# Kernel optimization log

Hardware: AMD Instinct MI355X
Metric: run time of the kernel (lower is better)

Reference implementation:

```python
import jax, jax.numpy as jnp
import numpy as np

B, T, S, D, H, DK, DV, DFF = 2, 2048, 2048, 1024, 16, 64, 64, 4096
EPS = 1e-5


def layer_norm(x, g, b):
    m = jnp.mean(x, axis=-1, keepdims=True)
    v = jnp.var(x, axis=-1, keepdims=True)
    return (x - m) * jax.lax.rsqrt(v + EPS) * g + b


def mha(q_in, k_in, v_in, Wq, bq, Wk, bk, Wv, bv, Wo, bo, mask):
    # q_in: [B, Lq, D]; k_in/v_in: [B, Lk, D]
    Q = (q_in @ Wq + bq).reshape(q_in.shape[0], -1, H, DK).transpose(0, 2, 1, 3)  # [B,H,Lq,dk]
    K = (k_in @ Wk + bk).reshape(k_in.shape[0], -1, H, DK).transpose(0, 2, 1, 3)
    V = (v_in @ Wv + bv).reshape(v_in.shape[0], -1, H, DV).transpose(0, 2, 1, 3)
    scores = jnp.einsum('bhqd,bhkd->bhqk', Q, K) / jnp.float32(np.sqrt(DK))
    scores = jnp.where(mask == 0, jnp.float32(-1e9), scores)
    attn = jax.nn.softmax(scores, axis=-1)
    out = jnp.einsum('bhqk,bhkd->bhqd', attn, V)
    out = out.transpose(0, 2, 1, 3).reshape(q_in.shape[0], -1, H * DV)
    return out @ Wo + bo


def setup_inputs() -> dict:
    key = jax.random.key(0)
    ks = jax.random.split(key, 16)
    s = 0.02
    inp = {
        'x': jax.random.normal(ks[0], (B, T, D), jnp.float32),
        'encoder_output': jax.random.normal(ks[1], (B, S, D), jnp.float32),
        'lookahead_mask': jnp.tril(jnp.ones((T, T), jnp.int32))[None, None],  # [1,1,T,T]
        'padding_mask': jnp.ones((1, 1, 1, S), jnp.int32),
        # self-attention params
        'sa_Wq': jax.random.normal(ks[2], (D, H * DK), jnp.float32) * s,
        'sa_bq': jnp.zeros((H * DK,), jnp.float32),
        'sa_Wk': jax.random.normal(ks[3], (D, H * DK), jnp.float32) * s,
        'sa_bk': jnp.zeros((H * DK,), jnp.float32),
        'sa_Wv': jax.random.normal(ks[4], (D, H * DV), jnp.float32) * s,
        'sa_bv': jnp.zeros((H * DV,), jnp.float32),
        'sa_Wo': jax.random.normal(ks[5], (H * DV, D), jnp.float32) * s,
        'sa_bo': jnp.zeros((D,), jnp.float32),
        # cross-attention params
        'ca_Wq': jax.random.normal(ks[6], (D, H * DK), jnp.float32) * s,
        'ca_bq': jnp.zeros((H * DK,), jnp.float32),
        'ca_Wk': jax.random.normal(ks[7], (D, H * DK), jnp.float32) * s,
        'ca_bk': jnp.zeros((H * DK,), jnp.float32),
        'ca_Wv': jax.random.normal(ks[8], (D, H * DV), jnp.float32) * s,
        'ca_bv': jnp.zeros((H * DV,), jnp.float32),
        'ca_Wo': jax.random.normal(ks[9], (H * DV, D), jnp.float32) * s,
        'ca_bo': jnp.zeros((D,), jnp.float32),
        # feed-forward params
        'ff_W1': jax.random.normal(ks[10], (D, DFF), jnp.float32) * s,
        'ff_b1': jnp.zeros((DFF,), jnp.float32),
        'ff_W2': jax.random.normal(ks[11], (DFF, D), jnp.float32) * s,
        'ff_b2': jnp.zeros((D,), jnp.float32),
        # layer norms
        'ln1_g': jnp.ones((D,), jnp.float32), 'ln1_b': jnp.zeros((D,), jnp.float32),
        'ln2_g': jnp.ones((D,), jnp.float32), 'ln2_b': jnp.zeros((D,), jnp.float32),
        'ln3_g': jnp.ones((D,), jnp.float32), 'ln3_b': jnp.zeros((D,), jnp.float32),
    }
    return inp


def reference(x, encoder_output, lookahead_mask, padding_mask,
              sa_Wq, sa_bq, sa_Wk, sa_bk, sa_Wv, sa_bv, sa_Wo, sa_bo,
              ca_Wq, ca_bq, ca_Wk, ca_bk, ca_Wv, ca_bv, ca_Wo, ca_bo,
              ff_W1, ff_b1, ff_W2, ff_b2,
              ln1_g, ln1_b, ln2_g, ln2_b, ln3_g, ln3_b):
    attn1 = mha(x, x, x, sa_Wq, sa_bq, sa_Wk, sa_bk, sa_Wv, sa_bv, sa_Wo, sa_bo, lookahead_mask)
    addnorm1 = layer_norm(x + attn1, ln1_g, ln1_b)
    attn2 = mha(addnorm1, encoder_output, encoder_output,
                ca_Wq, ca_bq, ca_Wk, ca_bk, ca_Wv, ca_bv, ca_Wo, ca_bo, padding_mask)
    addnorm2 = layer_norm(addnorm1 + attn2, ln2_g, ln2_b)
    ff = jax.nn.relu(addnorm2 @ ff_W1 + ff_b1) @ ff_W2 + ff_b2
    return layer_norm(addnorm2 + ff, ln3_g, ln3_b)
```

## Files before the change

### kernel.cpp

```cpp
#include <hip/hip_runtime.h>

typedef unsigned short u16;
typedef unsigned int   u32;
typedef __attribute__((ext_vector_type(8)))  __bf16 bf16x8;
typedef __attribute__((ext_vector_type(4)))  float  f32x4;
typedef __attribute__((ext_vector_type(16))) float  f32x16;
typedef __attribute__((ext_vector_type(4)))  unsigned short u16x4;

#define DEV static __device__ __forceinline__

DEV u16 cvt_bf16(float f){
  u32 u = __builtin_bit_cast(u32, f);
  u32 r = (u + 0x7FFFu + ((u >> 16) & 1u)) >> 16;
  return (u16)r;
}

typedef __attribute__((address_space(1))) void* as1p;
typedef __attribute__((address_space(3))) void* as3p;

DEV void gld16(void* lds, const void* g){
  __builtin_amdgcn_global_load_lds((as1p)g, (as3p)lds, 16, 0, 0);
}

DEV f32x4 mfma16(bf16x8 a, bf16x8 b, f32x4 c){
  return __builtin_amdgcn_mfma_f32_16x16x32_bf16(a, b, c, 0, 0, 0);
}
DEV f32x16 mfma32(bf16x8 a, bf16x8 b, f32x16 c){
  return __builtin_amdgcn_mfma_f32_32x32x16_bf16(a, b, c, 0, 0, 0);
}

DEV bf16x8 ld8(const u16* p){ return *(const bf16x8*)p; }

DEV u32 cvtpk(float lo, float hi){
  u32 r; asm("v_cvt_pk_bf16_f32 %0, %1, %2" : "=v"(r) : "v"(lo), "v"(hi)); return r;
}
DEV void perm32swap(u32 &a, u32 &b){
  asm("v_permlane32_swap_b32 %0, %1" : "+v"(a), "+v"(b));
}
DEV bf16x8 frag4(u32 w0,u32 w1,u32 w2,u32 w3){
  union{ u32 w[4]; bf16x8 f; } u; u.w[0]=w0; u.w[1]=w1; u.w[2]=w2; u.w[3]=w3; return u.f;
}

DEV int swz64(int row, int blk){ return row*64 + ((blk ^ (row & 7)) << 3); }
DEV int swz32(int row, int blk){ return row*32 + ((blk ^ (row & 3)) << 3); }

__global__ __launch_bounds__(256) void castk(const float* __restrict__ in,
                                             u16* __restrict__ out, int n4){
  int i = blockIdx.x*256 + threadIdx.x;
  if(i >= n4) return;
  f32x4 v = *(const f32x4*)(in + (size_t)i*4);
  u16x4 o;
  #pragma unroll
  for(int j=0;j<4;j++) o[j] = cvt_bf16(v[j]);
  *(u16x4*)(out + (size_t)i*4) = o;
}

__global__ __launch_bounds__(256) void fcopy(const float* __restrict__ s,
                                             float* __restrict__ d, int n){
  int i = blockIdx.x*256 + threadIdx.x;
  if(i < n) d[i] = s[i];
}

__global__ __launch_bounds__(256) void maskbias(const int* __restrict__ pm,
                                                float* __restrict__ bias, int n){
  int i = blockIdx.x*256 + threadIdx.x;
  if(i < n) bias[i] = pm[i] ? 0.f : -8e9f;
}

__global__ __launch_bounds__(256) void wcast_t(const float* __restrict__ W,
                                               u16* __restrict__ Wt, int K, int N){
  __shared__ u16 tile[64][66];
  const int k0 = blockIdx.x*64, n0 = blockIdx.y*64;
  const int lr = threadIdx.x >> 4, c4 = (threadIdx.x & 15)*4;
  #pragma unroll
  for(int p=0;p<4;p++){
    const int r = lr + p*16;
    f32x4 v = *(const f32x4*)&W[(size_t)(k0+r)*N + n0 + c4];
    #pragma unroll
    for(int j=0;j<4;j++) tile[r][c4+j] = cvt_bf16(v[j]);
  }
  __syncthreads();
  #pragma unroll
  for(int p=0;p<4;p++){
    const int n = lr + p*16;
    u16x4 u;
    #pragma unroll
    for(int j=0;j<4;j++) u[j] = tile[c4+j][n];
    *(u16x4*)&Wt[(size_t)(n0+n)*K + k0 + c4] = u;
  }
}

__global__ __launch_bounds__(256) void vtrans(const u16* __restrict__ V,
                                              u16* __restrict__ Vt, int L, int ld){
  __shared__ u16 tile[64][66];
  const int t0 = blockIdx.x*64;
  const int h = blockIdx.y, b = blockIdx.z;
  const int lr = threadIdx.x >> 4, c4 = (threadIdx.x & 15)*4;
  #pragma unroll
  for(int p=0;p<4;p++){
    const int r = lr + p*16;
    u16x4 v = *(const u16x4*)&V[(size_t)(b*L + t0 + r)*ld + h*64 + c4];
    #pragma unroll
    for(int j=0;j<4;j++) tile[r][c4+j] = v[j];
  }
  __syncthreads();
  #pragma unroll
  for(int p=0;p<4;p++){
    const int d = lr + p*16;
    u16x4 u;
    #pragma unroll
    for(int j=0;j<4;j++) u[j] = tile[c4+j][d];
    *(u16x4*)&Vt[((size_t)((b*16 + h)*64 + d))*L + t0 + c4] = u;
  }
}

template<int OMODE, int BN>
__global__ __launch_bounds__(256, BN==128 ? 3 : 4) void gemm_bt(
    const u16* __restrict__ A, const u16* __restrict__ Bt,
    const float* __restrict__ bias, void* __restrict__ Cout,
    int N, int K)
{
  __shared__ __align__(16) u16 As[2][128*32];
  __shared__ __align__(16) u16 Bs[2][BN*32];
  constexpr int NJ = BN/32;
  const int tid = threadIdx.x, wave = tid>>6, lane = tid&63;
  const int fr = lane&15, fg = lane>>4;
  const int bm = blockIdx.x*128, bn = blockIdx.y*BN;
  const int wm = (wave>>1)*64, wn = (wave&1)*(BN/2);
  const f32x4 z4 = {0.f,0.f,0.f,0.f};
  f32x4 acc[4][NJ];
  #pragma unroll
  for(int i=0;i<4;i++)
    #pragma unroll
    for(int j=0;j<NJ;j++) acc[i][j] = z4;

  const int srA = wave*32 + (lane>>2);
  const int cl_l = (lane&3)*8;
  const int cl_g = ((lane&3) ^ ((lane>>2)&3))*8;
  const int srB = (BN==128) ? srA : (wave*16 + (lane>>2));
  const u16* gA = A  + (size_t)(bm + srA)*K + cl_g;
  const u16* gB = Bt + (size_t)(bn + srB)*K + cl_g;

  auto stage = [&](int p, int ko){
    u16* lA = &As[p][srA*32 + cl_l];
    u16* lB = &Bs[p][srB*32 + cl_l];
    gld16(lA,     gA + ko);
    gld16(lA+512, gA + ko + (size_t)16*K);
    gld16(lB,     gB + ko);
    if(BN==128) gld16(lB+512, gB + ko + (size_t)16*K);
  };

  const int nk = K >> 5;
  stage(0, 0);
  __syncthreads();
  for(int kt=0; kt<nk; ++kt){
    const int cur = kt & 1;
    if(kt+1 < nk) stage(cur^1, (kt+1)*32);
    bf16x8 af[4], bfv[NJ];
    #pragma unroll
    for(int i=0;i<4;i++) af[i] = ld8(&As[cur][swz32(wm + i*16 + fr, fg)]);
    #pragma unroll
    for(int j=0;j<NJ;j++) bfv[j] = ld8(&Bs[cur][swz32(wn + j*16 + fr, fg)]);
    __builtin_amdgcn_s_setprio(1);
    #pragma unroll
    for(int i=0;i<4;i++)
      #pragma unroll
      for(int j=0;j<NJ;j++)
        acc[i][j] = mfma16(af[i], bfv[j], acc[i][j]);
    __builtin_amdgcn_s_setprio(0);
    __syncthreads();
  }

  const int r0 = bm + wm + fg*4;
  const int c0 = bn + wn + fr;
  #pragma unroll
  for(int j=0;j<NJ;j++){
    const int col = c0 + j*16;
    const float bv = bias[col];
    #pragma unroll
    for(int i=0;i<4;i++){
      #pragma unroll
      for(int r=0;r<4;r++){
        const float v = acc[i][j][r] + bv;
        const size_t idx = (size_t)(r0 + i*16 + r)*N + col;
        if(OMODE==0)      ((float*)Cout)[idx] = v;
        else if(OMODE==1) ((u16*)Cout)[idx]   = cvt_bf16(v);
        else              ((u16*)Cout)[idx]   = cvt_bf16(fmaxf(v, 0.f));
      }
    }
  }
}

template<bool CAUSAL>
__global__ __launch_bounds__(256,2) void attn2(
    const u16* __restrict__ Qg, int ldq, const u16* __restrict__ Kg, int ldk,
    const u16* __restrict__ Vt, const float* __restrict__ biasg,
    u16* __restrict__ Og, int Lk)
{
  __shared__ __align__(16) u16 Ks[2][64*64];
  __shared__ __align__(16) u16 Vs[2][64*64];
  const int tid = threadIdx.x, wave = tid>>6, lane = tid&63;
  const int l31 = lane&31, hi = lane>>5;
  const int bid = blockIdx.x;
  const int g   = (bid&7)*4 + ((bid>>3)>>4);
  const int qb  = (bid>>3)&15;
  const int h = g&15, b = g>>4;
  const int qi = CAUSAL ? ((qb&1) ? (15-(qb>>1)) : (qb>>1)) : qb;
  const int q0 = qi*128;
  const int qw = q0 + wave*32;
  const int qrow = qw + l31;

  bf16x8 qf[4];
  {
    const u16* Qp = Qg + (size_t)(b*2048 + qrow)*ldq + h*64;
    #pragma unroll
    for(int c=0;c<4;c++) qf[c] = ld8(Qp + c*16 + hi*8);
  }

  f32x16 o0, o1;
  #pragma unroll
  for(int r=0;r<16;r++){ o0[r]=0.f; o1[r]=0.f; }
  float m = -3e38f, lsum = 0.f;

  const int srow = wave*16 + (lane>>3);
  const int cl_l = (lane&7)*8;
  const int cl_g = ((lane&7) ^ ((lane>>3)&7))*8;
  const u16* Kp = Kg + (size_t)(b*2048 + srow)*ldk + h*64 + cl_g;
  const u16* Vp = Vt + ((size_t)((b*16 + h)*64 + srow))*Lk + cl_g;

  auto stage = [&](int p, int kv0){
    u16* lK = &Ks[p][srow*64 + cl_l];
    u16* lV = &Vs[p][srow*64 + cl_l];
    gld16(lK,     Kp + (size_t)kv0*ldk);
    gld16(lK+512, Kp + (size_t)(kv0+8)*ldk);
    gld16(lV,     Vp + kv0);
    gld16(lV+512, Vp + kv0 + 8*(size_t)Lk);
  };

  const int nkt = CAUSAL ? ((q0+128)>>6) : (Lk>>6);

  stage(0, 0);
  __syncthreads();
  for(int kt=0; kt<nkt; ++kt){
    const int cur = kt & 1;
    const int kv0 = kt*64;
    if(kt+1 < nkt) stage(cur^1, (kt+1)*64);

    if(!CAUSAL || kv0 <= qw+31){
      f32x16 s0, s1;
      #pragma unroll
      for(int r=0;r<16;r++){ s0[r]=0.f; s1[r]=0.f; }
      __builtin_amdgcn_s_setprio(1);
      #pragma unroll
      for(int c=0;c<4;c++){
        bf16x8 k0 = ld8(&Ks[cur][swz64(l31,      2*c+hi)]);
        bf16x8 k1 = ld8(&Ks[cur][swz64(32 + l31, 2*c+hi)]);
        s0 = mfma32(k0, qf[c], s0);
        s1 = mfma32(k1, qf[c], s1);
      }
      __builtin_amdgcn_s_setprio(0);

      float p[32];
      #pragma unroll
      for(int r=0;r<16;r++){ p[r]=s0[r]; p[16+r]=s1[r]; }

      if(CAUSAL){
        if(kv0 + 63 > qw){
          #pragma unroll
          for(int n=0;n<2;n++)
            #pragma unroll
            for(int r=0;r<16;r++){
              const int kc = kv0 + 32*n + (r&3) + 8*(r>>2) + 4*hi;
              if(kc > qrow) p[16*n+r] = -8e9f;
            }
        }
      } else {
        #pragma unroll
        for(int n=0;n<2;n++)
          #pragma unroll
          for(int cq=0;cq<4;cq++){
            f32x4 bv = *(const f32x4*)&biasg[kv0 + 32*n + 8*cq + 4*hi];
            #pragma unroll
            for(int i=0;i<4;i++) p[16*n+4*cq+i] += bv[i];
          }
      }

      float pm = p[0];
      #pragma unroll
      for(int r=1;r<32;r++) pm = fmaxf(pm, p[r]);
      pm = fmaxf(pm, __shfl_xor(pm, 32));
      if(__any(pm > m + 8.f)){
        const float nm = fmaxf(m, pm);
        const float fac = __expf((m - nm)*0.125f);
        lsum *= fac;
        #pragma unroll
        for(int r=0;r<16;r++){
          const int qidx = (r&3) + 8*(r>>2) + 4*hi;
          const float fb = __builtin_bit_cast(float,
              __builtin_amdgcn_ds_bpermute(qidx<<2, __builtin_bit_cast(int, fac)));
          o0[r] *= fb; o1[r] *= fb;
        }
        m = nm;
      }
      const float ms = m*0.125f;
      float rs = 0.f;
      #pragma unroll
      for(int r=0;r<32;r++){ p[r] = __expf(p[r]*0.125f - ms); rs += p[r]; }
      rs += __shfl_xor(rs, 32);
      lsum += rs;

      u32 pw[16];
      #pragma unroll
      for(int n=0;n<2;n++)
        #pragma unroll
        for(int cp=0;cp<2;cp++){
          const int base = 16*n + 8*cp, cc = 2*n + cp;
          u32 a1 = cvtpk(p[base+0], p[base+1]);
          u32 a2 = cvtpk(p[base+2], p[base+3]);
          u32 b1 = cvtpk(p[base+4], p[base+5]);
          u32 b2 = cvtpk(p[base+6], p[base+7]);
          perm32swap(a1, b1);
          perm32swap(a2, b2);
          pw[4*cc+0]=a1; pw[4*cc+1]=a2; pw[4*cc+2]=b1; pw[4*cc+3]=b2;
        }

      __builtin_amdgcn_s_setprio(1);
      #pragma unroll
      for(int cc=0;cc<4;cc++){
        bf16x8 pf = frag4(pw[4*cc], pw[4*cc+1], pw[4*cc+2], pw[4*cc+3]);
        bf16x8 v0 = ld8(&Vs[cur][swz64(l31,      2*cc+hi)]);
        bf16x8 v1 = ld8(&Vs[cur][swz64(32 + l31, 2*cc+hi)]);
        o0 = mfma32(pf, v0, o0);
        o1 = mfma32(pf, v1, o1);
      }
      __builtin_amdgcn_s_setprio(0);
    }
    __syncthreads();
  }

  const float invl = 1.f / lsum;
  u16* Op = Og + (size_t)(b*2048 + qw)*1024 + h*64;
  #pragma unroll
  for(int r=0;r<16;r++){
    const int qidx = (r&3) + 8*(r>>2) + 4*hi;
    const float il = __builtin_bit_cast(float,
        __builtin_amdgcn_ds_bpermute(qidx<<2, __builtin_bit_cast(int, invl)));
    Op[(size_t)qidx*1024 + l31]      = cvt_bf16(o0[r]*il);
    Op[(size_t)qidx*1024 + 32 + l31] = cvt_bf16(o1[r]*il);
  }
}

__global__ __launch_bounds__(256) void add_ln(const float* __restrict__ X,
                        const float* __restrict__ Dl,
                        const float* __restrict__ gam, const float* __restrict__ bet,
                        float* __restrict__ outf, u16* __restrict__ outb){
  __shared__ float red[8];
  const int tid = threadIdx.x, wave = tid>>6, lane = tid&63;
  const size_t base = ((size_t)blockIdx.x << 10) + tid*4;
  f32x4 xv = *(const f32x4*)(X + base);
  f32x4 dv = *(const f32x4*)(Dl + base);
  f32x4 v;
  #pragma unroll
  for(int j=0;j<4;j++) v[j] = xv[j] + dv[j];
  float s = v[0]+v[1]+v[2]+v[3];
  float q = v[0]*v[0]+v[1]*v[1]+v[2]*v[2]+v[3]*v[3];
  #pragma unroll
  for(int off=1;off<64;off<<=1){ s += __shfl_xor(s,off); q += __shfl_xor(q,off); }
  if(lane==0){ red[wave]=s; red[4+wave]=q; }
  __syncthreads();
  s = red[0]+red[1]+red[2]+red[3];
  q = red[4]+red[5]+red[6]+red[7];
  const float mean = s*(1.f/1024.f);
  const float var  = q*(1.f/1024.f) - mean*mean;
  const float rr = rsqrtf(var + 1e-5f);
  const int c = tid*4;
  f32x4 y;
  #pragma unroll
  for(int j=0;j<4;j++) y[j] = (v[j]-mean)*rr*gam[c+j] + bet[c+j];
  *(f32x4*)(outf + base) = y;
  if(outb){
    u16x4 ob;
    #pragma unroll
    for(int j=0;j<4;j++) ob[j] = cvt_bf16(y[j]);
    *(u16x4*)(outb + base) = ob;
  }
}

extern "C" void kernel_launch(void* const* d_in, const int* in_sizes, int n_in,
                              void* d_out, int out_size, void* d_ws, size_t ws_size,
                              hipStream_t stream)
{
  (void)in_sizes; (void)n_in; (void)out_size; (void)ws_size;
  const float* x    = (const float*)d_in[0];
  const float* enc  = (const float*)d_in[1];
  const int*   pmask= (const int*)d_in[3];
  const float* saWq = (const float*)d_in[4];  const float* sabq = (const float*)d_in[5];
  const float* saWk = (const float*)d_in[6];  const float* sabk = (const float*)d_in[7];
  const float* saWv = (const float*)d_in[8];  const float* sabv = (const float*)d_in[9];
  const float* saWo = (const float*)d_in[10]; const float* sabo = (const float*)d_in[11];
  const float* caWq = (const float*)d_in[12]; const float* cabq = (const float*)d_in[13];
  const float* caWk = (const float*)d_in[14]; const float* cabk = (const float*)d_in[15];
  const float* caWv = (const float*)d_in[16]; const float* cabv = (const float*)d_in[17];
  const float* caWo = (const float*)d_in[18]; const float* cabo = (const float*)d_in[19];
  const float* fW1  = (const float*)d_in[20]; const float* fb1  = (const float*)d_in[21];
  const float* fW2  = (const float*)d_in[22]; const float* fb2  = (const float*)d_in[23];
  const float* l1g  = (const float*)d_in[24]; const float* l1b  = (const float*)d_in[25];
  const float* l2g  = (const float*)d_in[26]; const float* l2b  = (const float*)d_in[27];
  const float* l3g  = (const float*)d_in[28]; const float* l3b  = (const float*)d_in[29];

  char* wsp = (char*)d_ws;
  size_t off = 0;
  auto take = [&](size_t bytes)->void*{ void* p = wsp + off; off += (bytes + 255) & ~(size_t)255; return p; };
  u16* slotA  = (u16*)take(8388608);
  u16* Encb   = (u16*)take(8388608);
  u16* WqkvT  = (u16*)take(6291456);
  u16* cWqT   = (u16*)take(2097152);
  u16* cWkvT  = (u16*)take(4194304);
  u16* WoT    = (u16*)take(2097152);
  u16* cWoT   = (u16*)take(2097152);
  u16* W1T    = (u16*)take(8388608);
  u16* W2T    = (u16*)take(8388608);
  float* bqkv = (float*)take(16384);
  float* bkvc = (float*)take(16384);
  float* biasg= (float*)take(16384);
  u16* slotB  = (u16*)take(25165824);
  u16* Vtb    = (u16*)take(8388608);
  u16* Ob     = (u16*)take(8388608);
  u16* an1b   = (u16*)take(8388608);
  float* projf= (float*)take(16777216);
  float* an1f = (float*)take(16777216);
  float* an2f = (float*)take(16777216);
  u16* ffh    = (u16*)take(33554432);
  u16* Xbf = slotA;  u16* Qcb = slotA;  u16* an2b = slotA;
  u16* QKVb = slotB; u16* KVc = slotB;

  castk<<<4096,256,0,stream>>>(x,   Xbf,  1048576);
  castk<<<4096,256,0,stream>>>(enc, Encb, 1048576);
  wcast_t<<<dim3(16,16),256,0,stream>>>(saWq, WqkvT,                1024, 1024);
  wcast_t<<<dim3(16,16),256,0,stream>>>(saWk, WqkvT + 1024*1024,    1024, 1024);
  wcast_t<<<dim3(16,16),256,0,stream>>>(saWv, WqkvT + 2*1024*1024,  1024, 1024);
  wcast_t<<<dim3(16,16),256,0,stream>>>(saWo, WoT, 1024, 1024);
  wcast_t<<<dim3(16,16),256,0,stream>>>(caWq, cWqT, 1024, 1024);
  wcast_t<<<dim3(16,16),256,0,stream>>>(caWk, cWkvT,               1024, 1024);
  wcast_t<<<dim3(16,16),256,0,stream>>>(caWv, cWkvT + 1024*1024,   1024, 1024);
  wcast_t<<<dim3(16,16),256,0,stream>>>(caWo, cWoT, 1024, 1024);
  wcast_t<<<dim3(16,64),256,0,stream>>>(fW1, W1T, 1024, 4096);
  wcast_t<<<dim3(64,16),256,0,stream>>>(fW2, W2T, 4096, 1024);
  fcopy<<<4,256,0,stream>>>(sabq, bqkv,        1024);
  fcopy<<<4,256,0,stream>>>(sabk, bqkv + 1024, 1024);
  fcopy<<<4,256,0,stream>>>(sabv, bqkv + 2048, 1024);
  fcopy<<<4,256,0,stream>>>(cabk, bkvc,        1024);
  fcopy<<<4,256,0,stream>>>(cabv, bkvc + 1024, 1024);
  maskbias<<<8,256,0,stream>>>(pmask, biasg, 2048);

  gemm_bt<1,128><<<dim3(32,24),256,0,stream>>>(Xbf, WqkvT, bqkv, QKVb, 3072, 1024);
  vtrans<<<dim3(32,16,2),256,0,stream>>>(QKVb + 2048, Vtb, 2048, 3072);
  attn2<true><<<512,256,0,stream>>>(QKVb, 3072, QKVb + 1024, 3072, Vtb, nullptr, Ob, 2048);
  gemm_bt<0,64><<<dim3(32,16),256,0,stream>>>(Ob, WoT, sabo, projf, 1024, 1024);
  add_ln<<<4096,256,0,stream>>>(x, projf, l1g, l1b, an1f, an1b);

  gemm_bt<1,64><<<dim3(32,16),256,0,stream>>>(an1b, cWqT, cabq, Qcb, 1024, 1024);
  gemm_bt<1,128><<<dim3(32,16),256,0,stream>>>(Encb, cWkvT, bkvc, KVc, 2048, 1024);
  vtrans<<<dim3(32,16,2),256,0,stream>>>(KVc + 1024, Vtb, 2048, 2048);
  attn2<false><<<512,256,0,stream>>>(Qcb, 1024, KVc, 2048, Vtb, biasg, Ob, 2048);
  gemm_bt<0,64><<<dim3(32,16),256,0,stream>>>(Ob, cWoT, cabo, projf, 1024, 1024);
  add_ln<<<4096,256,0,stream>>>(an1f, projf, l2g, l2b, an2f, an2b);

  gemm_bt<2,128><<<dim3(32,32),256,0,stream>>>(an2b, W1T, fb1, ffh, 4096, 1024);
  gemm_bt<0,64><<<dim3(32,16),256,0,stream>>>(ffh, W2T, fb2, projf, 1024, 4096);
  add_ln<<<4096,256,0,stream>>>(an2f, projf, l3g, l3b, (float*)d_out, nullptr);
}
```

Measured before the change: 460.1 us.

## Split attention KV range in two and merge partial results in a combine kernel

```diff
diff --git a/kernel.cpp b/kernel.cpp
--- a/kernel.cpp
+++ b/kernel.cpp
@@ -9,6 +9,8 @@
 
 #define DEV static __device__ __forceinline__
 
+#define SC 0.1803368801111243f
+
 DEV u16 cvt_bf16(float f){
   u32 u = __builtin_bit_cast(u32, f);
   u32 r = (u + 0x7FFFu + ((u >> 16) & 1u)) >> 16;
@@ -30,6 +32,10 @@
 }
 
 DEV bf16x8 ld8(const u16* p){ return *(const bf16x8*)p; }
+
+DEV float vexp2(float x){
+  float y; asm("v_exp_f32 %0, %1" : "=v"(y) : "v"(x)); return y;
+}
 
 DEV u32 cvtpk(float lo, float hi){
   u32 r; asm("v_cvt_pk_bf16_f32 %0, %1, %2" : "=v"(r) : "v"(lo), "v"(hi)); return r;
@@ -192,18 +198,21 @@
 }
 
 template<bool CAUSAL>
-__global__ __launch_bounds__(256,2) void attn2(
+__global__ __launch_bounds__(256,4) void attn3(
     const u16* __restrict__ Qg, int ldq, const u16* __restrict__ Kg, int ldk,
     const u16* __restrict__ Vt, const float* __restrict__ biasg,
-    u16* __restrict__ Og, int Lk)
+    float* __restrict__ Opart, float* __restrict__ Ml, float* __restrict__ Ll,
+    int Lk)
 {
   __shared__ __align__(16) u16 Ks[2][64*64];
   __shared__ __align__(16) u16 Vs[2][64*64];
+  __shared__ float FacL[4][32];
   const int tid = threadIdx.x, wave = tid>>6, lane = tid&63;
   const int l31 = lane&31, hi = lane>>5;
   const int bid = blockIdx.x;
-  const int g   = (bid&7)*4 + ((bid>>3)>>4);
-  const int qb  = (bid>>3)&15;
+  const int g    = (bid&7)*4 + (bid>>8);
+  const int r5   = (bid>>3)&31;
+  const int part = r5&1, qb = r5>>1;
   const int h = g&15, b = g>>4;
   const int qi = CAUSAL ? ((qb&1) ? (15-(qb>>1)) : (qb>>1)) : qb;
   const int q0 = qi*128;
@@ -237,14 +246,15 @@
     gld16(lV+512, Vp + kv0 + 8*(size_t)Lk);
   };
 
-  const int nkt = CAUSAL ? ((q0+128)>>6) : (Lk>>6);
-
-  stage(0, 0);
+  const int span = CAUSAL ? (qi+1) : ((Lk>>6)>>1);
+  const int t0 = part*span, t1 = t0 + span;
+
+  stage(0, t0*64);
   __syncthreads();
-  for(int kt=0; kt<nkt; ++kt){
-    const int cur = kt & 1;
+  for(int kt=t0; kt<t1; ++kt){
+    const int cur = (kt-t0)&1;
     const int kv0 = kt*64;
-    if(kt+1 < nkt) stage(cur^1, (kt+1)*64);
+    if(kt+1 < t1) stage(cur^1, (kt+1)*64);
 
     if(!CAUSAL || kv0 <= qw+31){
       f32x16 s0, s1;
@@ -289,23 +299,22 @@
       #pragma unroll
       for(int r=1;r<32;r++) pm = fmaxf(pm, p[r]);
       pm = fmaxf(pm, __shfl_xor(pm, 32));
-      if(__any(pm > m + 8.f)){
+      if(__any(pm > m + 64.f)){
         const float nm = fmaxf(m, pm);
-        const float fac = __expf((m - nm)*0.125f);
+        const float fac = vexp2((m - nm)*SC);
         lsum *= fac;
+        FacL[wave][l31] = fac;
         #pragma unroll
         for(int r=0;r<16;r++){
           const int qidx = (r&3) + 8*(r>>2) + 4*hi;
-          const float fb = __builtin_bit_cast(float,
-              __builtin_amdgcn_ds_bpermute(qidx<<2, __builtin_bit_cast(int, fac)));
+          const float fb = FacL[wave][qidx];
           o0[r] *= fb; o1[r] *= fb;
         }
         m = nm;
       }
-      const float ms = m*0.125f;
       float rs = 0.f;
       #pragma unroll
-      for(int r=0;r<32;r++){ p[r] = __expf(p[r]*0.125f - ms); rs += p[r]; }
+      for(int r=0;r<32;r++){ p[r] = vexp2((p[r]-m)*SC); rs += p[r]; }
       rs += __shfl_xor(rs, 32);
       lsum += rs;
 
@@ -338,16 +347,39 @@
     __syncthreads();
   }
 
-  const float invl = 1.f / lsum;
-  u16* Op = Og + (size_t)(b*2048 + qw)*1024 + h*64;
+  float* Op = Opart + (size_t)part*4194304 + (size_t)(b*2048 + qw)*1024 + h*64;
   #pragma unroll
   for(int r=0;r<16;r++){
     const int qidx = (r&3) + 8*(r>>2) + 4*hi;
-    const float il = __builtin_bit_cast(float,
-        __builtin_amdgcn_ds_bpermute(qidx<<2, __builtin_bit_cast(int, invl)));
-    Op[(size_t)qidx*1024 + l31]      = cvt_bf16(o0[r]*il);
-    Op[(size_t)qidx*1024 + 32 + l31] = cvt_bf16(o1[r]*il);
-  }
+    Op[(size_t)qidx*1024 + l31]      = o0[r];
+    Op[(size_t)qidx*1024 + 32 + l31] = o1[r];
+  }
+  if(hi==0){
+    const int mi = part*65536 + (b*2048 + qw + l31)*16 + h;
+    Ml[mi] = m; Ll[mi] = lsum;
+  }
+}
+
+__global__ __launch_bounds__(256) void att_combine(
+    const float* __restrict__ O0, const float* __restrict__ O1,
+    const float* __restrict__ Ml, const float* __restrict__ Ll,
+    u16* __restrict__ Ob)
+{
+  const int row = blockIdx.x, tid = threadIdx.x;
+  const int h = tid>>4;
+  const int mi = row*16 + h;
+  const float m0 = Ml[mi], m1 = Ml[65536+mi];
+  const float l0 = Ll[mi], l1 = Ll[65536+mi];
+  const float mx = fmaxf(m0, m1);
+  const float w0 = vexp2((m0-mx)*SC), w1 = vexp2((m1-mx)*SC);
+  const float inv = 1.f/(w0*l0 + w1*l1);
+  const size_t base = (size_t)row*1024 + tid*4;
+  f32x4 a = *(const f32x4*)(O0 + base);
+  f32x4 c = *(const f32x4*)(O1 + base);
+  u16x4 o;
+  #pragma unroll
+  for(int j=0;j<4;j++) o[j] = cvt_bf16((w0*a[j] + w1*c[j])*inv);
+  *(u16x4*)(Ob + base) = o;
 }
 
 __global__ __launch_bounds__(256) void add_ln(const float* __restrict__ X,
@@ -430,9 +462,13 @@
   float* projf= (float*)take(16777216);
   float* an1f = (float*)take(16777216);
   float* an2f = (float*)take(16777216);
-  u16* ffh    = (u16*)take(33554432);
+  char* ffhb  = (char*)take(33554432);
   u16* Xbf = slotA;  u16* Qcb = slotA;  u16* an2b = slotA;
   u16* QKVb = slotB; u16* KVc = slotB;
+  u16* ffh   = (u16*)ffhb;
+  float* Opar = (float*)ffhb;
+  float* Mlb = (float*)an1b;
+  float* Llb = Mlb + 131072;
 
   castk<<<4096,256,0,stream>>>(x,   Xbf,  1048576);
   castk<<<4096,256,0,stream>>>(enc, Encb, 1048576);
@@ -455,14 +491,18 @@
 
   gemm_bt<1,128><<<dim3(32,24),256,0,stream>>>(Xbf, WqkvT, bqkv, QKVb, 3072, 1024);
   vtrans<<<dim3(32,16,2),256,0,stream>>>(QKVb + 2048, Vtb, 2048, 3072);
-  attn2<true><<<512,256,0,stream>>>(QKVb, 3072, QKVb + 1024, 3072, Vtb, nullptr, Ob, 2048);
+  attn3<true><<<1024,256,0,stream>>>(QKVb, 3072, QKVb + 1024, 3072, Vtb, nullptr,
+                                     Opar, Mlb, Llb, 2048);
+  att_combine<<<4096,256,0,stream>>>(Opar, Opar + 4194304, Mlb, Llb, Ob);
   gemm_bt<0,64><<<dim3(32,16),256,0,stream>>>(Ob, WoT, sabo, projf, 1024, 1024);
   add_ln<<<4096,256,0,stream>>>(x, projf, l1g, l1b, an1f, an1b);
 
   gemm_bt<1,64><<<dim3(32,16),256,0,stream>>>(an1b, cWqT, cabq, Qcb, 1024, 1024);
   gemm_bt<1,128><<<dim3(32,16),256,0,stream>>>(Encb, cWkvT, bkvc, KVc, 2048, 1024);
   vtrans<<<dim3(32,16,2),256,0,stream>>>(KVc + 1024, Vtb, 2048, 2048);
-  attn2<false><<<512,256,0,stream>>>(Qcb, 1024, KVc, 2048, Vtb, biasg, Ob, 2048);
+  attn3<false><<<1024,256,0,stream>>>(Qcb, 1024, KVc, 2048, Vtb, biasg,
+                                      Opar, Mlb, Llb, 2048);
+  att_combine<<<4096,256,0,stream>>>(Opar, Opar + 4194304, Mlb, Llb, Ob);
   gemm_bt<0,64><<<dim3(32,16),256,0,stream>>>(Ob, cWoT, cabo, projf, 1024, 1024);
   add_ln<<<4096,256,0,stream>>>(an1f, projf, l2g, l2b, an2f, an2b);
 
```

Result: no change. 454.2 us (-1.3%).
